# Performance work log

Measured on AMD Instinct MI355X. Metric: run time of the kernel, lower is better.

## Reference

```python
import jax, jax.numpy as jnp
import numpy as np
import math


def get_alibi_slopes(n_heads: int) -> np.ndarray:
    # Bloom-style ALiBi slopes.
    cp2 = 2 ** math.floor(math.log2(n_heads))
    base = 2.0 ** (-(2.0 ** -(math.log2(cp2) - 3)))
    slopes = base ** np.arange(1, cp2 + 1, dtype=np.float32)
    if cp2 != n_heads:
        extra_base = 2.0 ** (-(2.0 ** -(math.log2(2 * cp2) - 3)))
        extra = extra_base ** np.arange(1, 2 * (n_heads - cp2) + 1, 2, dtype=np.float32)
        slopes = np.concatenate([slopes, extra])
    return slopes.astype(np.float32)


def setup_inputs() -> dict:
    key = jax.random.key(0)
    k1, k2, k3 = jax.random.split(key, 3)
    B, S, D, H = 2, 2048, 2048, 16
    T = B * S
    return {
        "hidden_states": jax.random.normal(k1, (T, D), dtype=jnp.float32) * 0.02,
        "qkv_weight": jax.random.normal(k2, (3, D, D), dtype=jnp.float32) * 0.02,
        "o_proj_weight": jax.random.normal(k3, (D, D), dtype=jnp.float32) * 0.02,
        "batch": B,
        "seq_len": S,
        "n_heads": H,
    }


def reference(hidden_states, qkv_weight, o_proj_weight, batch, seq_len, n_heads):
    T, D = hidden_states.shape
    head_dim = D // n_heads
    sm_scale = 1.0 / math.sqrt(head_dim)
    slopes = jnp.asarray(get_alibi_slopes(n_heads))  # [H]

    # QKV projection: equivalent of bmm(hidden.expand(3,-1,-1), qkv_weight)
    qkv = jnp.einsum("td,cde->cte", hidden_states, qkv_weight)  # [3, T, D]
    q, k, v = qkv.reshape(3, batch, seq_len, n_heads, head_dim)

    # Varlen causal attention with ALiBi (prefill / context phase).
    scores = jnp.einsum("bqhd,bkhd->bhqk", q, k) * sm_scale  # [B,H,S,S]
    pos = jnp.arange(seq_len)
    rel = (pos[None, :] - pos[:, None]).astype(jnp.float32)  # k_idx - q_idx
    scores = scores + slopes[None, :, None, None] * rel[None, None]
    causal = pos[None, :] <= pos[:, None]  # [S,S]
    scores = jnp.where(causal[None, None], scores, jnp.finfo(scores.dtype).min)
    probs = jax.nn.softmax(scores, axis=-1)
    attn = jnp.einsum("bhqk,bkhd->bqhd", probs, v)  # [B,S,H,Dh]

    attn = attn.reshape(T, D)
    return attn @ o_proj_weight
```

## Files before the change

kernel.cpp:

```cpp
#include <hip/hip_runtime.h>
#include <math.h>
#include <stdint.h>

typedef __bf16 bf16x8_t __attribute__((ext_vector_type(8)));
typedef float  f32x4_t  __attribute__((ext_vector_type(4)));
typedef unsigned short u16;


__device__ __forceinline__ u16 f2bf(float f) {
  unsigned u = __float_as_uint(f);
  u += 0x7FFFu + ((u >> 16) & 1u);
  return (u16)(u >> 16);
}

__device__ __forceinline__ void gload_lds16(const u16* gsrc, u16* ldst) {
  __builtin_amdgcn_global_load_lds(
      (__attribute__((address_space(1))) void*)(const_cast<u16*>(gsrc)),
      (__attribute__((address_space(3))) void*)(ldst),
      16, 0, 0);
}

__device__ __forceinline__ int sw8(int row, int e) { return e ^ ((row & 7) << 3); }

__device__ __forceinline__ void store_out(float* C, long idx, float v) { C[idx] = v; }
__device__ __forceinline__ void store_out(u16* C, long idx, float v) { C[idx] = f2bf(v); }

__device__ __forceinline__ float alibi_slope(int h, int H) {
  int cp2 = 1, lg = 0;
  while (cp2 * 2 <= H) { cp2 *= 2; lg++; }
  if (h < cp2) {
    double e = exp2((double)-(lg - 3));
    return (float)exp2(-e * (double)(h + 1));
  } else {
    double e = exp2((double)-(lg + 1 - 3));
    return (float)exp2(-e * (double)(2 * (h - cp2) + 1));
  }
}


__global__ __launch_bounds__(256) void k_cast_bf16(const float* __restrict__ in,
                                                   u16* __restrict__ out, long n) {
  long i = ((long)blockIdx.x * 256 + threadIdx.x) * 4;
  if (i + 3 < n) {
    float4 v = *reinterpret_cast<const float4*>(in + i);
    ushort4 o;
    o.x = f2bf(v.x); o.y = f2bf(v.y); o.z = f2bf(v.z); o.w = f2bf(v.w);
    *reinterpret_cast<ushort4*>(out + i) = o;
  }
}


__global__ __launch_bounds__(256) void k_transpose_cast(const float* __restrict__ in,
                                                        u16* __restrict__ out,
                                                        int R, int C) {
  __shared__ float tile[32][33];
  const float* inz = in + (long)blockIdx.z * R * C;
  u16* outz = out + (long)blockIdx.z * R * C;
  const int tx = threadIdx.x & 31, ty = threadIdx.x >> 5;
  const int r0 = blockIdx.y * 32, c0 = blockIdx.x * 32;
#pragma unroll
  for (int i = 0; i < 4; ++i)
    tile[ty + i * 8][tx] = inz[(long)(r0 + ty + i * 8) * C + c0 + tx];
  __syncthreads();
#pragma unroll
  for (int i = 0; i < 4; ++i)
    outz[(long)(c0 + ty + i * 8) * R + r0 + tx] = f2bf(tile[tx][ty + i * 8]);
}


__global__ __launch_bounds__(256) void k_transpose_v(const u16* __restrict__ V,
                                                     u16* __restrict__ Vt,
                                                     int S, int D, int Dh, int H) {
  __shared__ u16 tile[32][33];
  const int bh = blockIdx.z, b = bh / H, h = bh % H;
  const int tx = threadIdx.x & 31, ty = threadIdx.x >> 5;
  const int s0 = blockIdx.x * 32, d0 = blockIdx.y * 32;
  const u16* vin = V + (long)b * S * D + (long)h * Dh;
#pragma unroll
  for (int i = 0; i < 4; ++i)
    tile[ty + i * 8][tx] = vin[(long)(s0 + ty + i * 8) * D + d0 + tx];
  __syncthreads();
  u16* vout = Vt + (long)bh * Dh * S;
#pragma unroll
  for (int i = 0; i < 4; ++i)
    vout[(long)(d0 + ty + i * 8) * S + s0 + tx] = tile[tx][ty + i * 8];
}


template <typename OUT_T>
__global__ __launch_bounds__(256) void k_gemm_bt(const u16* __restrict__ A,
                                                 const u16* __restrict__ Bt,
                                                 OUT_T* __restrict__ C,
                                                 int M, int N, int K,
                                                 long strideA, long strideB, long strideC) {
  __shared__ u16 As[128][64];
  __shared__ u16 Bs[128][64];
  const int tid = threadIdx.x;
  const int wid = tid >> 6, lane = tid & 63;
  const int wr = wid >> 1, wc = wid & 1;

  A  += (long)blockIdx.z * strideA;
  Bt += (long)blockIdx.z * strideB;
  C  += (long)blockIdx.z * strideC;

  const long abase = (long)blockIdx.y * 128;
  const long bbase = (long)blockIdx.x * 128;

  f32x4_t acc[4][4];
#pragma unroll
  for (int m = 0; m < 4; ++m)
#pragma unroll
    for (int n = 0; n < 4; ++n)
#pragma unroll
      for (int r = 0; r < 4; ++r) acc[m][n][r] = 0.f;

  const int srow = lane >> 3;
  const int scol = (lane & 7) * 8;

  for (int kt = 0; kt < K; kt += 64) {
    __syncthreads();
#pragma unroll
    for (int i = 0; i < 4; ++i) {
      const int lr = i * 32 + wid * 8;
      gload_lds16(A  + (abase + lr + srow) * (long)K + kt + scol, &As[lr][0]);
      gload_lds16(Bt + (bbase + lr + srow) * (long)K + kt + scol, &Bs[lr][0]);
    }
    __syncthreads();

    const int frow = lane & 15;
    const int fk8  = (lane >> 4) * 8;
#pragma unroll
    for (int kk = 0; kk < 2; ++kk) {
      bf16x8_t af[4], bfr[4];
#pragma unroll
      for (int m = 0; m < 4; ++m)
        af[m] = *reinterpret_cast<const bf16x8_t*>(&As[wr * 64 + m * 16 + frow][kk * 32 + fk8]);
#pragma unroll
      for (int n = 0; n < 4; ++n)
        bfr[n] = *reinterpret_cast<const bf16x8_t*>(&Bs[wc * 64 + n * 16 + frow][kk * 32 + fk8]);
#pragma unroll
      for (int m = 0; m < 4; ++m)
#pragma unroll
        for (int n = 0; n < 4; ++n)
          acc[m][n] = __builtin_amdgcn_mfma_f32_16x16x32_bf16(af[m], bfr[n], acc[m][n], 0, 0, 0);
    }
  }

  const int orow = (lane >> 4) * 4;
  const int ocol = lane & 15;
#pragma unroll
  for (int m = 0; m < 4; ++m)
#pragma unroll
    for (int n = 0; n < 4; ++n)
#pragma unroll
      for (int r = 0; r < 4; ++r) {
        const long row = abase + wr * 64 + m * 16 + orow + r;
        const long col = bbase + wc * 64 + n * 16 + ocol;
        store_out(C, row * (long)N + col, acc[m][n][r]);
      }
}


__global__ __launch_bounds__(256) void k_attn(const u16* __restrict__ Q,
                                              const u16* __restrict__ Kb,
                                              const u16* __restrict__ Vt,
                                              u16* __restrict__ Out,
                                              int B, int S, int H, int D, float sm_scale) {
  __shared__ u16 Ks[64][128];
  __shared__ u16 Vs[128][64];
  __shared__ u16 Ps[128][64];

  const int tid = threadIdx.x, wid = tid >> 6, lane = tid & 63;

  const int nq = gridDim.x, nbh = gridDim.y;
  const int lin = blockIdx.x + nq * blockIdx.y;
  const int qb0 = lin / nbh;
  const int bh  = lin % nbh;
  const int qb  = (qb0 < nq / 2) ? qb0 : (nq + nq / 2 - 1 - qb0);

  const int b = bh / H, h = bh % H;
  const int Dh = D / H;

  const float slope = alibi_slope(h, H);
  const long qrow0 = (long)b * S + qb * 128 + wid * 32;

  const int frow = lane & 15;
  const int fk8  = (lane >> 4) * 8;
  const int orow = (lane >> 4) * 4;
  const int ocol = lane & 15;

  bf16x8_t aq[2][4];
#pragma unroll
  for (int m = 0; m < 2; ++m)
#pragma unroll
    for (int kk = 0; kk < 4; ++kk)
      aq[m][kk] = *reinterpret_cast<const bf16x8_t*>(
          Q + (qrow0 + m * 16 + frow) * (long)D + h * Dh + kk * 32 + fk8);

  f32x4_t oacc[2][8];
#pragma unroll
  for (int m = 0; m < 2; ++m)
#pragma unroll
    for (int no = 0; no < 8; ++no)
#pragma unroll
      for (int r = 0; r < 4; ++r) oacc[m][no][r] = 0.f;

  float mrun[2][4], lrun[2][4];
#pragma unroll
  for (int m = 0; m < 2; ++m)
#pragma unroll
    for (int r = 0; r < 4; ++r) { mrun[m][r] = -3.0e38f; lrun[m][r] = 0.f; }

  const int qg0 = qb * 128 + wid * 32;
  const int ktiles = 2 * qb + 2;

  for (int kt = 0; kt < ktiles; ++kt) {
    __syncthreads();
#pragma unroll
    for (int i = 0; i < 4; ++i) {
      const int lr = i * 16 + wid * 4;
      const int r  = lr + (lane >> 4);
      gload_lds16(Kb + ((long)b * S + kt * 64 + r) * (long)D + h * Dh + sw8(r, (lane & 15) * 8),
                  &Ks[lr][0]);
    }
#pragma unroll
    for (int i = 0; i < 4; ++i) {
      const int lr = i * 32 + wid * 8;
      const int r  = lr + (lane >> 3);
      gload_lds16(Vt + ((long)bh * Dh + r) * (long)S + kt * 64 + sw8(r, (lane & 7) * 8),
                  &Vs[lr][0]);
    }
    __syncthreads();

    const bool active = (kt * 64) <= (qg0 + 31);

    if (active) {
      f32x4_t sacc[2][4];
#pragma unroll
      for (int m = 0; m < 2; ++m)
#pragma unroll
        for (int n = 0; n < 4; ++n)
#pragma unroll
          for (int r = 0; r < 4; ++r) sacc[m][n][r] = 0.f;

#pragma unroll
      for (int kk = 0; kk < 4; ++kk) {
        bf16x8_t bk[4];
#pragma unroll
        for (int n = 0; n < 4; ++n) {
          const int krow = n * 16 + frow;
          bk[n] = *reinterpret_cast<const bf16x8_t*>(&Ks[krow][sw8(krow, kk * 32 + fk8)]);
        }
#pragma unroll
        for (int m = 0; m < 2; ++m)
#pragma unroll
          for (int n = 0; n < 4; ++n)
            sacc[m][n] = __builtin_amdgcn_mfma_f32_16x16x32_bf16(aq[m][kk], bk[n], sacc[m][n], 0, 0, 0);
      }

      float tmax[2][4];
#pragma unroll
      for (int m = 0; m < 2; ++m)
#pragma unroll
        for (int r = 0; r < 4; ++r) tmax[m][r] = -3.0e38f;

#pragma unroll
      for (int m = 0; m < 2; ++m)
#pragma unroll
        for (int n = 0; n < 4; ++n)
#pragma unroll
          for (int r = 0; r < 4; ++r) {
            const int qg = qg0 + m * 16 + orow + r;
            const int kg = kt * 64 + n * 16 + ocol;
            float v = sacc[m][n][r] * sm_scale + slope * (float)(kg - qg);
            v = (kg <= qg) ? v : -1.0e30f;
            sacc[m][n][r] = v;
            tmax[m][r] = fmaxf(tmax[m][r], v);
          }
#pragma unroll
      for (int m = 0; m < 2; ++m)
#pragma unroll
        for (int r = 0; r < 4; ++r) {
          float t = tmax[m][r];
          t = fmaxf(t, __shfl_xor(t, 1));
          t = fmaxf(t, __shfl_xor(t, 2));
          t = fmaxf(t, __shfl_xor(t, 4));
          t = fmaxf(t, __shfl_xor(t, 8));
          tmax[m][r] = t;
        }

      float tsum[2][4];
#pragma unroll
      for (int m = 0; m < 2; ++m)
#pragma unroll
        for (int r = 0; r < 4; ++r) {
          const float mnew = fmaxf(mrun[m][r], tmax[m][r]);
          const float alpha = __expf(mrun[m][r] - mnew);
          mrun[m][r] = mnew;
          lrun[m][r] *= alpha;
#pragma unroll
          for (int no = 0; no < 8; ++no) oacc[m][no][r] *= alpha;
          tsum[m][r] = 0.f;
        }
#pragma unroll
      for (int m = 0; m < 2; ++m)
#pragma unroll
        for (int n = 0; n < 4; ++n)
#pragma unroll
          for (int r = 0; r < 4; ++r) {
            const float p = __expf(sacc[m][n][r] - mrun[m][r]);
            tsum[m][r] += p;
            const int prow = wid * 32 + m * 16 + orow + r;
            Ps[prow][sw8(prow, n * 16 + ocol)] = f2bf(p);
          }
#pragma unroll
      for (int m = 0; m < 2; ++m)
#pragma unroll
        for (int r = 0; r < 4; ++r) {
          float t = tsum[m][r];
          t += __shfl_xor(t, 1);
          t += __shfl_xor(t, 2);
          t += __shfl_xor(t, 4);
          t += __shfl_xor(t, 8);
          lrun[m][r] += t;
        }
    }

    __syncthreads();

    if (active) {
#pragma unroll
      for (int kk = 0; kk < 2; ++kk) {
        bf16x8_t pa[2];
        const int prow0 = wid * 32 + frow;
        const int prow1 = wid * 32 + 16 + frow;
        pa[0] = *reinterpret_cast<const bf16x8_t*>(&Ps[prow0][sw8(prow0, kk * 32 + fk8)]);
        pa[1] = *reinterpret_cast<const bf16x8_t*>(&Ps[prow1][sw8(prow1, kk * 32 + fk8)]);
#pragma unroll
        for (int no = 0; no < 8; ++no) {
          const int vrow = no * 16 + frow;
          bf16x8_t bv = *reinterpret_cast<const bf16x8_t*>(&Vs[vrow][sw8(vrow, kk * 32 + fk8)]);
          oacc[0][no] = __builtin_amdgcn_mfma_f32_16x16x32_bf16(pa[0], bv, oacc[0][no], 0, 0, 0);
          oacc[1][no] = __builtin_amdgcn_mfma_f32_16x16x32_bf16(pa[1], bv, oacc[1][no], 0, 0, 0);
        }
      }
    }
  }

#pragma unroll
  for (int m = 0; m < 2; ++m)
#pragma unroll
    for (int r = 0; r < 4; ++r) {
      const float rl = 1.0f / lrun[m][r];
      const long trow = qrow0 + m * 16 + orow + r;
#pragma unroll
      for (int no = 0; no < 8; ++no)
        Out[trow * (long)D + h * Dh + no * 16 + ocol] = f2bf(oacc[m][no][r] * rl);
    }
}


extern "C" void kernel_launch(void* const* d_in, const int* in_sizes, int n_in,
                              void* d_out, int out_size, void* d_ws, size_t ws_size,
                              hipStream_t stream) {
  const float* hs   = (const float*)d_in[0];
  const float* qkvw = (const float*)d_in[1];
  const float* ow   = (const float*)d_in[2];

  const int D = 2048, B = 2, H = 16;
  const long TD = (long)in_sizes[0];
  const long DD = (long)in_sizes[2];
  const int T = (int)(TD / D);
  const int S = T / B;
  const int Dh = D / H;
  const float sm_scale = 1.0f / sqrtf((float)Dh);

  u16* ws  = (u16*)d_ws;
  u16* hsb = ws;
  u16* wt  = ws + TD;
  u16* owt = wt + 3 * DD;
  u16* qkv = owt + DD;
  u16* vt   = wt;
  u16* attn = hsb;

  k_cast_bf16<<<dim3((unsigned)(TD / 1024)), 256, 0, stream>>>(hs, hsb, TD);
  k_transpose_cast<<<dim3(D / 32, D / 32, 3), 256, 0, stream>>>(qkvw, wt, D, D);
  k_transpose_cast<<<dim3(D / 32, D / 32, 1), 256, 0, stream>>>(ow, owt, D, D);
  k_gemm_bt<u16><<<dim3(D / 128, T / 128, 3), 256, 0, stream>>>(
      hsb, wt, qkv, T, D, D, 0L, DD, TD);
  k_transpose_v<<<dim3(S / 32, Dh / 32, B * H), 256, 0, stream>>>(
      qkv + 2 * TD, vt, S, D, Dh, H);
  k_attn<<<dim3(S / 128, B * H), 256, 0, stream>>>(
      qkv, qkv + TD, vt, attn, B, S, H, D, sm_scale);
  k_gemm_bt<float><<<dim3(D / 128, T / 128, 1), 256, 0, stream>>>(
      attn, owt, (float*)d_out, T, D, D, 0L, 0L, 0L);
}
```

Measured before the change: 343.3 us.

## Replace GEMM with 256x256 double-buffered 8-wave kernel with XCD remap

Replaces the 128x128 single-buffered GEMM with a 512-thread 256x256-tile kernel. It double-buffers the LDS tiles, interleaves the next tile's global-to-LDS loads with MFMA phases, applies XOR-swizzled LDS layout, sets wave priority, and remaps workgroups across XCDs. The three QKV matrices are fused into one launch with N=3D, with column-based output routing. The goal is to hide memory latency and raise MFMA utilisation. In exchange it hardcodes a 2048 row stride and relies on delicate manual waitcnt and barrier sequencing.

```diff
diff --git a/kernel.cpp b/kernel.cpp
--- a/kernel.cpp
+++ b/kernel.cpp
@@ -37,6 +37,12 @@
   }
 }
 
+#define FENCE() asm volatile("" ::: "memory")
+#define BARRIER() do { FENCE(); __builtin_amdgcn_s_barrier(); \
+                       __builtin_amdgcn_sched_barrier(0); FENCE(); } while (0)
+#define WAITLGKM() do { asm volatile("s_waitcnt lgkmcnt(0)" ::: "memory"); \
+                        __builtin_amdgcn_sched_barrier(0); } while (0)
+
 
 __global__ __launch_bounds__(256) void k_cast_bf16(const float* __restrict__ in,
                                                    u16* __restrict__ out, long n) {
@@ -87,76 +93,160 @@
 }
 
 
+__device__ __forceinline__ void stage16(const u16* __restrict__ g, long grow0, int K,
+                                        int kt, int lr0, u16 (*lds)[64], int lane) {
+  const int e = (lane & 7) * 8;
+#pragma unroll
+  for (int i = 0; i < 2; ++i) {
+    const int r = lr0 + i * 8 + (lane >> 3);
+    gload_lds16(g + (grow0 + r) * (long)K + kt + (e ^ ((r & 7) << 3)), &lds[lr0 + i * 8][0]);
+  }
+}
+
 template <typename OUT_T>
-__global__ __launch_bounds__(256) void k_gemm_bt(const u16* __restrict__ A,
-                                                 const u16* __restrict__ Bt,
-                                                 OUT_T* __restrict__ C,
-                                                 int M, int N, int K,
-                                                 long strideA, long strideB, long strideC) {
-  __shared__ u16 As[128][64];
-  __shared__ u16 Bs[128][64];
-  const int tid = threadIdx.x;
-  const int wid = tid >> 6, lane = tid & 63;
-  const int wr = wid >> 1, wc = wid & 1;
-
-  A  += (long)blockIdx.z * strideA;
-  Bt += (long)blockIdx.z * strideB;
-  C  += (long)blockIdx.z * strideC;
-
-  const long abase = (long)blockIdx.y * 128;
-  const long bbase = (long)blockIdx.x * 128;
-
-  f32x4_t acc[4][4];
-#pragma unroll
-  for (int m = 0; m < 4; ++m)
+__global__ __launch_bounds__(512, 2) void k_gemm8(const u16* __restrict__ A,
+                                                  const u16* __restrict__ Bt,
+                                                  OUT_T* __restrict__ Cb,
+                                                  int M, int N, int K, long matStride) {
+  __shared__ u16 As[2][256][64];
+  __shared__ u16 Bs[2][256][64];
+
+  const int tid = threadIdx.x, wid = tid >> 6, lane = tid & 63;
+  const int wr = wid >> 2, wc = wid & 3;
+  const int frow = lane & 15, fk8 = (lane >> 4) * 8;
+  const int orow = (lane >> 4) * 4, ocol = lane & 15;
+
+  const int nwg = gridDim.x * gridDim.y;
+  const int orig = blockIdx.y * gridDim.x + blockIdx.x;
+  const int q = nwg >> 3, rr = nwg & 7;
+  const int xcd = orig & 7, sl = orig >> 3;
+  const int wg = (xcd < rr ? xcd * (q + 1) : rr * (q + 1) + (xcd - rr) * q) + sl;
+  const int by = wg / gridDim.x, bx = wg % gridDim.x;
+
+  const long abase = (long)by * 256, bbase = (long)bx * 256;
+
+  const int bg0 = (wid >> 1) * 64 + (wid & 1) * 16;
+  const int ag0 = (wid >> 2) * 128 + (wid & 3) * 16;
+
+  f32x4_t acc[8][4];
+#pragma unroll
+  for (int m = 0; m < 8; ++m)
 #pragma unroll
     for (int n = 0; n < 4; ++n)
 #pragma unroll
       for (int r = 0; r < 4; ++r) acc[m][n][r] = 0.f;
 
-  const int srow = lane >> 3;
-  const int scol = (lane & 7) * 8;
-
-  for (int kt = 0; kt < K; kt += 64) {
-    __syncthreads();
-#pragma unroll
-    for (int i = 0; i < 4; ++i) {
-      const int lr = i * 32 + wid * 8;
-      gload_lds16(A  + (abase + lr + srow) * (long)K + kt + scol, &As[lr][0]);
-      gload_lds16(Bt + (bbase + lr + srow) * (long)K + kt + scol, &Bs[lr][0]);
-    }
-    __syncthreads();
-
-    const int frow = lane & 15;
-    const int fk8  = (lane >> 4) * 8;
-#pragma unroll
-    for (int kk = 0; kk < 2; ++kk) {
-      bf16x8_t af[4], bfr[4];
-#pragma unroll
-      for (int m = 0; m < 4; ++m)
-        af[m] = *reinterpret_cast<const bf16x8_t*>(&As[wr * 64 + m * 16 + frow][kk * 32 + fk8]);
-#pragma unroll
-      for (int n = 0; n < 4; ++n)
-        bfr[n] = *reinterpret_cast<const bf16x8_t*>(&Bs[wc * 64 + n * 16 + frow][kk * 32 + fk8]);
-#pragma unroll
-      for (int m = 0; m < 4; ++m)
-#pragma unroll
-        for (int n = 0; n < 4; ++n)
-          acc[m][n] = __builtin_amdgcn_mfma_f32_16x16x32_bf16(af[m], bfr[n], acc[m][n], 0, 0, 0);
-    }
+  const int nt = K >> 6;
+
+  stage16(Bt, bbase, K, 0, bg0, Bs[0], lane);
+  stage16(Bt, bbase, K, 0, bg0 + 32, Bs[0], lane);
+  stage16(A, abase, K, 0, ag0, As[0], lane);
+  stage16(A, abase, K, 0, ag0 + 64, As[0], lane);
+  asm volatile("s_waitcnt vmcnt(2)" ::: "memory");
+  BARRIER();
+
+  bf16x8_t afr[4][2], bfr[4][2];
+  int cur = 0;
+
+  for (int t = 0; t < nt; ++t) {
+    const int ktn = (t + 1) << 6;
+    const bool hn = (t + 1 < nt);
+    const int nb = cur ^ 1;
+
+#pragma unroll
+    for (int m = 0; m < 4; ++m) {
+      const int r = wr * 128 + m * 16 + frow;
+      afr[m][0] = *reinterpret_cast<const bf16x8_t*>(&As[cur][r][sw8(r, fk8)]);
+      afr[m][1] = *reinterpret_cast<const bf16x8_t*>(&As[cur][r][sw8(r, 32 + fk8)]);
+    }
+#pragma unroll
+    for (int n = 0; n < 2; ++n) {
+      const int r = wc * 64 + n * 16 + frow;
+      bfr[n][0] = *reinterpret_cast<const bf16x8_t*>(&Bs[cur][r][sw8(r, fk8)]);
+      bfr[n][1] = *reinterpret_cast<const bf16x8_t*>(&Bs[cur][r][sw8(r, 32 + fk8)]);
+    }
+    if (hn) stage16(Bt, bbase, K, ktn, bg0, Bs[nb], lane);
+    BARRIER();
+    WAITLGKM();
+    __builtin_amdgcn_s_setprio(1);
+#pragma unroll
+    for (int m = 0; m < 4; ++m)
+#pragma unroll
+      for (int n = 0; n < 2; ++n) {
+        acc[m][n] = __builtin_amdgcn_mfma_f32_16x16x32_bf16(afr[m][0], bfr[n][0], acc[m][n], 0, 0, 0);
+        acc[m][n] = __builtin_amdgcn_mfma_f32_16x16x32_bf16(afr[m][1], bfr[n][1], acc[m][n], 0, 0, 0);
+      }
+    __builtin_amdgcn_s_setprio(0);
+    BARRIER();
+
+#pragma unroll
+    for (int n = 0; n < 2; ++n) {
+      const int r = wc * 64 + 32 + n * 16 + frow;
+      bfr[2 + n][0] = *reinterpret_cast<const bf16x8_t*>(&Bs[cur][r][sw8(r, fk8)]);
+      bfr[2 + n][1] = *reinterpret_cast<const bf16x8_t*>(&Bs[cur][r][sw8(r, 32 + fk8)]);
+    }
+    if (hn) stage16(Bt, bbase, K, ktn, bg0 + 32, Bs[nb], lane);
+    BARRIER();
+    WAITLGKM();
+    __builtin_amdgcn_s_setprio(1);
+#pragma unroll
+    for (int m = 0; m < 4; ++m)
+#pragma unroll
+      for (int n = 0; n < 2; ++n) {
+        acc[m][2 + n] = __builtin_amdgcn_mfma_f32_16x16x32_bf16(afr[m][0], bfr[2 + n][0], acc[m][2 + n], 0, 0, 0);
+        acc[m][2 + n] = __builtin_amdgcn_mfma_f32_16x16x32_bf16(afr[m][1], bfr[2 + n][1], acc[m][2 + n], 0, 0, 0);
+      }
+    __builtin_amdgcn_s_setprio(0);
+    if (hn) asm volatile("s_waitcnt vmcnt(4)" ::: "memory");
+    else    asm volatile("s_waitcnt vmcnt(0)" ::: "memory");
+    BARRIER();
+
+#pragma unroll
+    for (int m = 0; m < 4; ++m) {
+      const int r = wr * 128 + 64 + m * 16 + frow;
+      afr[m][0] = *reinterpret_cast<const bf16x8_t*>(&As[cur][r][sw8(r, fk8)]);
+      afr[m][1] = *reinterpret_cast<const bf16x8_t*>(&As[cur][r][sw8(r, 32 + fk8)]);
+    }
+    if (hn) stage16(A, abase, K, ktn, ag0, As[nb], lane);
+    BARRIER();
+    WAITLGKM();
+    __builtin_amdgcn_s_setprio(1);
+#pragma unroll
+    for (int m = 0; m < 4; ++m)
+#pragma unroll
+      for (int n = 0; n < 2; ++n) {
+        acc[4 + m][n] = __builtin_amdgcn_mfma_f32_16x16x32_bf16(afr[m][0], bfr[n][0], acc[4 + m][n], 0, 0, 0);
+        acc[4 + m][n] = __builtin_amdgcn_mfma_f32_16x16x32_bf16(afr[m][1], bfr[n][1], acc[4 + m][n], 0, 0, 0);
+      }
+    __builtin_amdgcn_s_setprio(0);
+    BARRIER();
+
+    if (hn) stage16(A, abase, K, ktn, ag0 + 64, As[nb], lane);
+    __builtin_amdgcn_s_setprio(1);
+#pragma unroll
+    for (int m = 0; m < 4; ++m)
+#pragma unroll
+      for (int n = 0; n < 2; ++n) {
+        acc[4 + m][2 + n] = __builtin_amdgcn_mfma_f32_16x16x32_bf16(afr[m][0], bfr[2 + n][0], acc[4 + m][2 + n], 0, 0, 0);
+        acc[4 + m][2 + n] = __builtin_amdgcn_mfma_f32_16x16x32_bf16(afr[m][1], bfr[2 + n][1], acc[4 + m][2 + n], 0, 0, 0);
+      }
+    __builtin_amdgcn_s_setprio(0);
+    if (hn) asm volatile("s_waitcnt vmcnt(2)" ::: "memory");
+    BARRIER();
+
+    cur ^= 1;
   }
 
-  const int orow = (lane >> 4) * 4;
-  const int ocol = lane & 15;
-#pragma unroll
-  for (int m = 0; m < 4; ++m)
+#pragma unroll
+  for (int m = 0; m < 8; ++m)
 #pragma unroll
     for (int n = 0; n < 4; ++n)
 #pragma unroll
       for (int r = 0; r < 4; ++r) {
-        const long row = abase + wr * 64 + m * 16 + orow + r;
-        const long col = bbase + wc * 64 + n * 16 + ocol;
-        store_out(C, row * (long)N + col, acc[m][n][r]);
+        const long row = abase + wr * 128 + m * 16 + orow + r;
+        const int col = (int)bbase + wc * 64 + n * 16 + ocol;
+        const long idx = (long)(col >> 11) * matStride + row * 2048 + (col & 2047);
+        store_out(Cb, idx, acc[m][n][r]);
       }
 }
 
@@ -386,12 +476,12 @@
   k_cast_bf16<<<dim3((unsigned)(TD / 1024)), 256, 0, stream>>>(hs, hsb, TD);
   k_transpose_cast<<<dim3(D / 32, D / 32, 3), 256, 0, stream>>>(qkvw, wt, D, D);
   k_transpose_cast<<<dim3(D / 32, D / 32, 1), 256, 0, stream>>>(ow, owt, D, D);
-  k_gemm_bt<u16><<<dim3(D / 128, T / 128, 3), 256, 0, stream>>>(
-      hsb, wt, qkv, T, D, D, 0L, DD, TD);
+  k_gemm8<u16><<<dim3((3 * D) / 256, T / 256), 512, 0, stream>>>(
+      hsb, wt, qkv, T, 3 * D, D, TD);
   k_transpose_v<<<dim3(S / 32, Dh / 32, B * H), 256, 0, stream>>>(
       qkv + 2 * TD, vt, S, D, Dh, H);
   k_attn<<<dim3(S / 128, B * H), 256, 0, stream>>>(
       qkv, qkv + TD, vt, attn, B, S, H, D, sm_scale);
-  k_gemm_bt<float><<<dim3(D / 128, T / 128, 1), 256, 0, stream>>>(
-      attn, owt, (float*)d_out, T, D, D, 0L, 0L, 0L);
-}
+  k_gemm8<float><<<dim3(D / 256, T / 256), 512, 0, stream>>>(
+      attn, owt, (float*)d_out, T, D, D, 0L);
+}
```

Measured after the change: 332.8 us. 3.1% less time.
